# Optimization experiments

Hardware: AMD Instinct MI355X
Metric: run time of the kernel (lower is better)

Reference implementation:

```python
import jax, jax.numpy as jnp
import numpy as np

TEMPERATURE = 0.07
N, D = 16384, 128
NUM_CLASSES = 100


def setup_inputs() -> dict:
    key = jax.random.key(0)
    kf, kl = jax.random.split(key)
    features = jax.random.normal(kf, (N, D), dtype=jnp.float32)
    labels = jax.random.randint(kl, (N,), 0, NUM_CLASSES, dtype=jnp.int64)
    return {"features": features, "labels": labels}


def reference(features, labels):
    # L2-normalize along feature dim (torch F.normalize, eps=1e-12)
    norm = jnp.linalg.norm(features, axis=1, keepdims=True)
    feats = features / jnp.maximum(norm, 1e-12)
    # [N, N] cosine similarity scaled by temperature
    sim = jnp.matmul(feats, feats.T) / TEMPERATURE
    # positive mask: same label, diagonal zeroed
    lab = labels.reshape(-1, 1)
    mask = (lab == lab.T).astype(sim.dtype)
    n = sim.shape[0]
    mask = mask * (1.0 - jnp.eye(n, dtype=sim.dtype))
    exp_sim = jnp.exp(sim)
    # denominator uses (1 - mask): all non-positive pairs INCLUDING the diagonal
    denom = jnp.sum(exp_sim * (1.0 - mask), axis=1)
    numer = jnp.sum(exp_sim * mask, axis=1)
    loss = -jnp.log(numer / denom + 1e-08)
    return jnp.mean(loss)
```

## Files before the change

kernel.cpp:

```cpp
#include <hip/hip_runtime.h>
#include <hip/hip_bf16.h>
#include <cstdint>
#include <cstddef>


#define N_ROWS 16384
#define DIM    128
#define TILE   128
#define NTILES (N_ROWS / TILE)

#define FEAT_SCALE 4.5398164f

typedef __attribute__((ext_vector_type(8))) short bf16x8;
typedef __attribute__((ext_vector_type(4))) float f32x4;

typedef const __attribute__((address_space(1))) unsigned int* gas_ptr;
typedef __attribute__((address_space(3))) unsigned int* las_ptr;

__global__ __launch_bounds__(256) void k_normalize(const float* __restrict__ F,
                                                   __hip_bfloat16* __restrict__ G) {
    int tid  = threadIdx.x;
    int lane = tid & 63;
    int wave = tid >> 6;
    int row  = blockIdx.x * 4 + wave;
    const float2* src = (const float2*)(F + (size_t)row * DIM) + lane;
    float2 x = *src;
    float s = x.x * x.x + x.y * x.y;
#pragma unroll
    for (int i = 1; i < 64; i <<= 1) s += __shfl_xor(s, i, 64);
    float scale = FEAT_SCALE / fmaxf(sqrtf(s), 1e-12f);
    __hip_bfloat162 h;
    h.x = __float2bfloat16(x.x * scale);
    h.y = __float2bfloat16(x.y * scale);
    ((__hip_bfloat162*)(G + (size_t)row * DIM))[lane] = h;
}

__global__ __launch_bounds__(256, 2) void k_tiles(const __hip_bfloat16* __restrict__ G,
                                                  const int* __restrict__ lab,
                                                  float* __restrict__ rN,
                                                  float* __restrict__ rT) {
    __shared__ __align__(16) char lds[65536 + 2048];
    float* sRed = (float*)(lds + 65536);

    int tid = threadIdx.x;

    int bid = blockIdx.x;
    int u = bid >> 2, i2 = bid & 3;
    int c = (int)((sqrtf(8.f * (float)u + 1.f) - 1.f) * 0.5f);
    while ((c + 1) * (c + 2) / 2 <= u) ++c;
    while (c * (c + 1) / 2 > u) --c;
    int g = u - c * (c + 1) / 2;
    int I = g * 4 + i2;
    int J0 = (I > c * 4) ? I : c * 4;
    int nj = c * 4 + 4 - J0;

    const char* gbase = (const char*)G;
    {
        const char* gA = gbase + (size_t)I * (TILE * DIM * 2);
        const char* gB = gbase + (size_t)J0 * (TILE * DIM * 2);
#pragma unroll
        for (int p = 0; p < 8; ++p) {
            int o = p * 4096 + tid * 16;
            int so = o ^ (((o >> 8) & 7) << 4);
            __builtin_amdgcn_global_load_lds((gas_ptr)(gA + so), (las_ptr)(lds + o), 16, 0, 0);
            __builtin_amdgcn_global_load_lds((gas_ptr)(gB + so), (las_ptr)(lds + 32768 + o), 16, 0, 0);
        }
    }

    int lane = tid & 63, w = tid >> 6;
    int wr = w >> 1, wc = w & 1;
    int lr = lane & 15, lhi = lane >> 4;

    __syncthreads();

    bf16x8 afr[4][4];
#pragma unroll
    for (int m = 0; m < 4; ++m) {
        int row = wr * 64 + m * 16 + lr;
#pragma unroll
        for (int kk = 0; kk < 4; ++kk) {
            int lin = row * 256 + kk * 64 + lhi * 16;
            afr[m][kk] = *(const bf16x8*)(lds + (lin ^ ((row & 7) << 4)));
        }
    }
    int rowbase = I * TILE + wr * 64;
    int labr[4][4];
#pragma unroll
    for (int m = 0; m < 4; ++m)
#pragma unroll
        for (int r = 0; r < 4; ++r) labr[m][r] = lab[rowbase + m * 16 + lhi * 4 + r];

    float rn[4][4], rt[4][4];
#pragma unroll
    for (int m = 0; m < 4; ++m)
#pragma unroll
        for (int r = 0; r < 4; ++r) { rn[m][r] = 0.f; rt[m][r] = 0.f; }

    __syncthreads();

    for (int t = 0; t < nj; ++t) {
        char* buf = lds + (((t & 1) ^ 1) << 15);
        int Jt = J0 + t;

        if (t + 1 < nj) {
            const char* gB = gbase + (size_t)(Jt + 1) * (TILE * DIM * 2);
            char* nbuf = lds + ((t & 1) << 15);
#pragma unroll
            for (int p = 0; p < 8; ++p) {
                int o = p * 4096 + tid * 16;
                int so = o ^ (((o >> 8) & 7) << 4);
                __builtin_amdgcn_global_load_lds((gas_ptr)(gB + so), (las_ptr)(nbuf + o), 16, 0, 0);
            }
        }
        __builtin_amdgcn_sched_barrier(0);

        int colbase = Jt * TILE + wc * 64;
        int labc[4];
#pragma unroll
        for (int n = 0; n < 4; ++n) labc[n] = lab[colbase + n * 16 + lr];

        f32x4 acc[4][4];
#pragma unroll
        for (int m = 0; m < 4; ++m)
#pragma unroll
            for (int n = 0; n < 4; ++n) acc[m][n] = (f32x4){0.f, 0.f, 0.f, 0.f};

#pragma unroll
        for (int kk = 0; kk < 4; ++kk) {
            bf16x8 b[4];
#pragma unroll
            for (int n = 0; n < 4; ++n) {
                int row = wc * 64 + n * 16 + lr;
                int lin = row * 256 + kk * 64 + lhi * 16;
                b[n] = *(const bf16x8*)(buf + (lin ^ ((row & 7) << 4)));
            }
#pragma unroll
            for (int m = 0; m < 4; ++m)
#pragma unroll
                for (int n = 0; n < 4; ++n)
                    acc[m][n] = __builtin_amdgcn_mfma_f32_16x16x32_bf16(afr[m][kk], b[n], acc[m][n], 0, 0, 0);
        }

        float cn[4] = {0.f, 0.f, 0.f, 0.f}, ct[4] = {0.f, 0.f, 0.f, 0.f};
        bool isdiag = (Jt == I);
        if (isdiag) {
#pragma unroll
            for (int n = 0; n < 4; ++n) {
                int col = colbase + n * 16 + lr;
#pragma unroll
                for (int m = 0; m < 4; ++m) {
                    int row0 = rowbase + m * 16 + lhi * 4;
#pragma unroll
                    for (int r = 0; r < 4; ++r) {
                        float e = __builtin_amdgcn_exp2f(acc[m][n][r]);
                        float te = ((row0 + r) != col) ? e : 0.f;
                        float me = (labr[m][r] == labc[n]) ? te : 0.f;
                        rn[m][r] += me;  rt[m][r] += te;
                        cn[n]    += me;  ct[n]    += te;
                    }
                }
            }
        } else {
#pragma unroll
            for (int n = 0; n < 4; ++n) {
#pragma unroll
                for (int m = 0; m < 4; ++m) {
#pragma unroll
                    for (int r = 0; r < 4; ++r) {
                        float e = __builtin_amdgcn_exp2f(acc[m][n][r]);
                        float me = (labr[m][r] == labc[n]) ? e : 0.f;
                        rn[m][r] += me;  rt[m][r] += e;
                        cn[n]    += me;  ct[n]    += e;
                    }
                }
            }
        }

#pragma unroll
        for (int n = 0; n < 4; ++n) {
            float v1 = cn[n], v2 = ct[n];
            v1 += __shfl_xor(v1, 16, 64); v1 += __shfl_xor(v1, 32, 64);
            v2 += __shfl_xor(v2, 16, 64); v2 += __shfl_xor(v2, 32, 64);
            if (lhi == 0) {
                int colt = wc * 64 + n * 16 + lr;
                sRed[wr * 128 + colt]       = v1;
                sRed[256 + wr * 128 + colt] = v2;
            }
        }
        __syncthreads();
        if (!isdiag && tid < 128) {
            float num = sRed[tid] + sRed[128 + tid];
            float tot = sRed[256 + tid] + sRed[384 + tid];
            int col = Jt * TILE + tid;
            atomicAdd(&rN[col], num);
            atomicAdd(&rT[col], tot);
        }
        __syncthreads();
    }

#pragma unroll
    for (int m = 0; m < 4; ++m)
#pragma unroll
        for (int r = 0; r < 4; ++r) {
            float v1 = rn[m][r], v2 = rt[m][r];
#pragma unroll
            for (int s = 1; s < 16; s <<= 1) {
                v1 += __shfl_xor(v1, s, 64);
                v2 += __shfl_xor(v2, s, 64);
            }
            if (lr == 0) {
                int rowt = wr * 64 + m * 16 + lhi * 4 + r;
                sRed[wc * 128 + rowt]       = v1;
                sRed[256 + wc * 128 + rowt] = v2;
            }
        }
    __syncthreads();
    if (tid < 128) {
        float num = sRed[tid] + sRed[128 + tid];
        float tot = sRed[256 + tid] + sRed[384 + tid];
        int row = I * TILE + tid;
        atomicAdd(&rN[row], num);
        atomicAdd(&rT[row], tot);
    }
}

__global__ __launch_bounds__(256) void k_rowloss(const float* __restrict__ rN,
                                                 const float* __restrict__ rT,
                                                 float* __restrict__ accum) {
    int row = blockIdx.x * 256 + threadIdx.x;
    float num = rN[row], tot = rT[row];
    float ediag = expf(14.285714285714286f);
    float denom = tot - num + ediag;
    float loss = -logf(num / denom + 1e-8f);
#pragma unroll
    for (int i = 1; i < 64; i <<= 1) loss += __shfl_xor(loss, i, 64);
    __shared__ float red[4];
    if ((threadIdx.x & 63) == 0) red[threadIdx.x >> 6] = loss;
    __syncthreads();
    if (threadIdx.x == 0)
        atomicAdd(accum, red[0] + red[1] + red[2] + red[3]);
}

__global__ void k_final(const float* __restrict__ accum, float* __restrict__ out) {
    out[0] = accum[0] / (float)N_ROWS;
}

extern "C" void kernel_launch(void* const* d_in, const int* in_sizes, int n_in,
                              void* d_out, int out_size, void* d_ws, size_t ws_size,
                              hipStream_t stream) {
    const float* F  = (const float*)d_in[0];
    const int* lab  = (const int*)d_in[1];
    float* out      = (float*)d_out;
    char* ws        = (char*)d_ws;

    __hip_bfloat16* G = (__hip_bfloat16*)ws;
    float* rN    = (float*)(ws + (4 << 20));
    float* rT    = rN + N_ROWS;
    float* accum = rT + N_ROWS;

    k_normalize<<<N_ROWS / 4, 256, 0, stream>>>(F, G);
    hipMemsetAsync(rN, 0, (size_t)N_ROWS * 2 * sizeof(float) + 16, stream);

    int nblocks = 2112;
    k_tiles<<<nblocks, 256, 0, stream>>>(G, lab, rN, rT);

    k_rowloss<<<N_ROWS / 256, 256, 0, stream>>>(rN, rT, accum);
    k_final<<<1, 1, 0, stream>>>(accum, out);
}
```

Measured before the change: 227.0 us.

## Replace global atomic row sums with per-chunk partial buffers and a reduce pass

```diff
diff --git a/kernel.cpp b/kernel.cpp
--- a/kernel.cpp
+++ b/kernel.cpp
@@ -8,6 +8,7 @@
 #define DIM    128
 #define TILE   128
 #define NTILES (N_ROWS / TILE)
+#define NCHUNK 32
 
 #define FEAT_SCALE 4.5398164f
 
@@ -35,10 +36,11 @@
     ((__hip_bfloat162*)(G + (size_t)row * DIM))[lane] = h;
 }
 
+template<bool ATOM>
 __global__ __launch_bounds__(256, 2) void k_tiles(const __hip_bfloat16* __restrict__ G,
                                                   const int* __restrict__ lab,
-                                                  float* __restrict__ rN,
-                                                  float* __restrict__ rT) {
+                                                  float2* __restrict__ pRow,
+                                                  float2* __restrict__ pCol) {
     __shared__ __align__(16) char lds[65536 + 2048];
     float* sRed = (float*)(lds + 65536);
 
@@ -189,11 +191,16 @@
         }
         __syncthreads();
         if (!isdiag && tid < 128) {
-            float num = sRed[tid] + sRed[128 + tid];
-            float tot = sRed[256 + tid] + sRed[384 + tid];
-            int col = Jt * TILE + tid;
-            atomicAdd(&rN[col], num);
-            atomicAdd(&rT[col], tot);
+            float2 v;
+            v.x = sRed[tid] + sRed[128 + tid];
+            v.y = sRed[256 + tid] + sRed[384 + tid];
+            if (ATOM) {
+                float* rN = (float*)pRow;  float* rT = (float*)pCol;
+                atomicAdd(&rN[Jt * TILE + tid], v.x);
+                atomicAdd(&rT[Jt * TILE + tid], v.y);
+            } else {
+                pCol[(size_t)I * N_ROWS + Jt * TILE + tid] = v;
+            }
         }
         __syncthreads();
     }
@@ -216,19 +223,39 @@
         }
     __syncthreads();
     if (tid < 128) {
-        float num = sRed[tid] + sRed[128 + tid];
-        float tot = sRed[256 + tid] + sRed[384 + tid];
-        int row = I * TILE + tid;
-        atomicAdd(&rN[row], num);
-        atomicAdd(&rT[row], tot);
-    }
-}
-
-__global__ __launch_bounds__(256) void k_rowloss(const float* __restrict__ rN,
-                                                 const float* __restrict__ rT,
-                                                 float* __restrict__ accum) {
+        float2 v;
+        v.x = sRed[tid] + sRed[128 + tid];
+        v.y = sRed[256 + tid] + sRed[384 + tid];
+        if (ATOM) {
+            float* rN = (float*)pRow;  float* rT = (float*)pCol;
+            atomicAdd(&rN[I * TILE + tid], v.x);
+            atomicAdd(&rT[I * TILE + tid], v.y);
+        } else {
+            pRow[(size_t)c * N_ROWS + I * TILE + tid] = v;
+        }
+    }
+}
+
+template<bool ATOM>
+__global__ __launch_bounds__(256) void k_reduce(const float2* __restrict__ pRow,
+                                                const float2* __restrict__ pCol,
+                                                float* __restrict__ accum) {
     int row = blockIdx.x * 256 + threadIdx.x;
-    float num = rN[row], tot = rT[row];
+    float num = 0.f, tot = 0.f;
+    if (ATOM) {
+        num = ((const float*)pRow)[row];
+        tot = ((const float*)pCol)[row];
+    } else {
+        int it = row >> 7;
+        for (int c = it >> 2; c < NCHUNK; ++c) {
+            float2 v = pRow[(size_t)c * N_ROWS + row];
+            num += v.x; tot += v.y;
+        }
+        for (int I = 0; I < it; ++I) {
+            float2 v = pCol[(size_t)I * N_ROWS + row];
+            num += v.x; tot += v.y;
+        }
+    }
     float ediag = expf(14.285714285714286f);
     float denom = tot - num + ediag;
     float loss = -logf(num / denom + 1e-8f);
@@ -254,16 +281,24 @@
     char* ws        = (char*)d_ws;
 
     __hip_bfloat16* G = (__hip_bfloat16*)ws;
-    float* rN    = (float*)(ws + (4 << 20));
-    float* rT    = rN + N_ROWS;
-    float* accum = rT + N_ROWS;
+    float* accum = (float*)(ws + ((size_t)4 << 20));
+    char* base   = ws + ((size_t)4 << 20) + 1024;
+    float2* pRow = (float2*)base;
+    float2* pCol = (float2*)(base + ((size_t)4 << 20));
 
     k_normalize<<<N_ROWS / 4, 256, 0, stream>>>(F, G);
-    hipMemsetAsync(rN, 0, (size_t)N_ROWS * 2 * sizeof(float) + 16, stream);
-
+    hipMemsetAsync(accum, 0, 16, stream);
+
+    size_t need = ((size_t)4 << 20) + 1024 + ((size_t)4 << 20) + ((size_t)16 << 20);
     int nblocks = 2112;
-    k_tiles<<<nblocks, 256, 0, stream>>>(G, lab, rN, rT);
-
-    k_rowloss<<<N_ROWS / 256, 256, 0, stream>>>(rN, rT, accum);
+    if (ws_size >= need) {
+        k_tiles<false><<<nblocks, 256, 0, stream>>>(G, lab, pRow, pCol);
+        k_reduce<false><<<N_ROWS / 256, 256, 0, stream>>>(pRow, pCol, accum);
+    } else {
+        hipMemsetAsync(pRow, 0, (size_t)N_ROWS * sizeof(float), stream);
+        hipMemsetAsync(pCol, 0, (size_t)N_ROWS * sizeof(float), stream);
+        k_tiles<true><<<nblocks, 256, 0, stream>>>(G, lab, pRow, pCol);
+        k_reduce<true><<<N_ROWS / 256, 256, 0, stream>>>(pRow, pCol, accum);
+    }
     k_final<<<1, 1, 0, stream>>>(accum, out);
 }
```

Result: slower. 248.6 us (+9.5%).
